# Optimization experiments

Measured on AMD Instinct MI355X. Metric: run time of the kernel, lower is better.

The kernel has to match this reference:

```python
import jax, jax.numpy as jnp
import numpy as np

B, L, D = 2048, 200, 128
ITEM_D, USER_D, CAT_D, DUR_D = 64, 64, 32, 16
N_USERS, N_ITEMS, N_CAT, N_DUR = 100000, 100000, 1000, 10
UDENSE, IDENSE = 25, 3
CONCAT = USER_D + ITEM_D + CAT_D + DUR_D + UDENSE + IDENSE + D  # 332
MLP1, MLP2 = 256, 128


def setup_inputs() -> dict:
    key = jax.random.key(0)
    ks = jax.random.split(key, 24)
    f = jax.random.normal
    hist_table = 0.01 * f(ks[0], (N_ITEMS + 1, D), dtype=jnp.float32)
    hist_table = hist_table.at[0].set(0.0)  # padding_idx=0
    return {
        'user_id': jax.random.randint(ks[1], (B,), 0, N_USERS, dtype=jnp.int32),
        'item_id': jax.random.randint(ks[2], (B,), 0, N_ITEMS, dtype=jnp.int32),
        'item_category': jax.random.randint(ks[3], (B,), 0, N_CAT, dtype=jnp.int32),
        'item_dur_bkt': jax.random.randint(ks[4], (B,), 0, N_DUR, dtype=jnp.int32),
        'history_seq': jax.random.randint(ks[5], (B, L), 0, N_ITEMS + 1, dtype=jnp.int32),
        'user_dense': f(ks[6], (B, UDENSE), dtype=jnp.float32),
        'item_dense': f(ks[7], (B, IDENSE), dtype=jnp.float32),
        'user_table': 0.01 * f(ks[8], (N_USERS, USER_D), dtype=jnp.float32),
        'item_table': 0.01 * f(ks[9], (N_ITEMS, ITEM_D), dtype=jnp.float32),
        'cat_table': 0.01 * f(ks[10], (N_CAT, CAT_D), dtype=jnp.float32),
        'dur_table': 0.01 * f(ks[11], (N_DUR, DUR_D), dtype=jnp.float32),
        'hist_table': hist_table,
        'target_proj_W': f(ks[12], (D, ITEM_D), dtype=jnp.float32) / np.sqrt(ITEM_D).astype(np.float32),
        'gru_Wi': f(ks[13], (3 * D, D), dtype=jnp.float32) / np.sqrt(D).astype(np.float32),
        'gru_Wh': f(ks[14], (3 * D, D), dtype=jnp.float32) / np.sqrt(D).astype(np.float32),
        'gru_bi': jnp.zeros((3 * D,), jnp.float32),
        'gru_bh': jnp.zeros((3 * D,), jnp.float32),
        'au_Wr': f(ks[15], (D, 2 * D), dtype=jnp.float32) / np.sqrt(2 * D).astype(np.float32),
        'au_br': jnp.zeros((D,), jnp.float32),
        'au_Wu': f(ks[16], (D, 2 * D), dtype=jnp.float32) / np.sqrt(2 * D).astype(np.float32),
        'au_bu': jnp.zeros((D,), jnp.float32),
        'au_Wh': f(ks[17], (D, 2 * D), dtype=jnp.float32) / np.sqrt(2 * D).astype(np.float32),
        'au_bh': jnp.zeros((D,), jnp.float32),
        'mlp_W1': f(ks[18], (MLP1, CONCAT), dtype=jnp.float32) / np.sqrt(CONCAT).astype(np.float32),
        'mlp_b1': jnp.zeros((MLP1,), jnp.float32),
        'mlp_W2': f(ks[19], (MLP2, MLP1), dtype=jnp.float32) / np.sqrt(MLP1).astype(np.float32),
        'mlp_b2': jnp.zeros((MLP2,), jnp.float32),
        'mlp_W3': f(ks[20], (1, MLP2), dtype=jnp.float32) / np.sqrt(MLP2).astype(np.float32),
        'mlp_b3': jnp.zeros((1,), jnp.float32),
    }


def _dien_fwd(user_id, item_id, item_category, item_dur_bkt, history_seq,
              user_dense, item_dense, user_table, item_table, cat_table,
              dur_table, hist_table, target_proj_W, gru_Wi, gru_Wh, gru_bi,
              gru_bh, au_Wr, au_br, au_Wu, au_bu, au_Wh, au_bh,
              mlp_W1, mlp_b1, mlp_W2, mlp_b2, mlp_W3, mlp_b3):
    mask = history_seq > 0                      # (B, L) bool, True = real item
    hist_emb = hist_table[history_seq]          # (B, L, D)

    # ---- InterestExtractor: torch nn.GRU (eval mode, dropout off) ----
    gi = jnp.einsum('bld,ed->ble', hist_emb, gru_Wi) + gru_bi  # (B, L, 3D)

    def gru_step(h, gi_t):
        gh = h @ gru_Wh.T + gru_bh
        i_r, i_z, i_n = jnp.split(gi_t, 3, axis=-1)
        h_r, h_z, h_n = jnp.split(gh, 3, axis=-1)
        r = jax.nn.sigmoid(i_r + h_r)
        z = jax.nn.sigmoid(i_z + h_z)
        n = jnp.tanh(i_n + r * h_n)
        h_new = (1.0 - z) * n + z * h
        return h_new, h_new

    h0 = jnp.zeros((hist_emb.shape[0], D), hist_emb.dtype)
    _, hs = jax.lax.scan(gru_step, h0, jnp.swapaxes(gi, 0, 1))
    h_states = jnp.swapaxes(hs, 0, 1)           # (B, L, D)

    # ---- Target-aware attention scores ----
    i_emb = item_table[item_id]                  # (B, ITEM_D)
    target = i_emb @ target_proj_W.T             # (B, D)
    scores = jnp.einsum('bld,bd->bl', h_states, target) / np.float32(np.sqrt(D))
    scores = jnp.where(mask, scores, jnp.float32(-1e9))
    attn = jax.nn.softmax(scores, axis=-1)       # (B, L)

    # ---- InterestEvolving: AUGRU scan over L timesteps ----
    def augru_step(h, inputs):
        x_t, e_t, m_t = inputs                   # (B,D), (B,), (B,)
        comb = jnp.concatenate([x_t, h], axis=-1)
        r = jax.nn.sigmoid(comb @ au_Wr.T + au_br)
        u = jax.nn.sigmoid(comb @ au_Wu.T + au_bu)
        u_prime = e_t[:, None] * u
        h_tilde = jnp.tanh(jnp.concatenate([x_t, r * h], axis=-1) @ au_Wh.T + au_bh)
        h_new = (1.0 - u_prime) * h + u_prime * h_tilde
        valid = m_t[:, None].astype(h.dtype)
        return valid * h_new + (1.0 - valid) * h, None

    xs = (jnp.swapaxes(h_states, 0, 1), attn.T, mask.T)
    evolved, _ = jax.lax.scan(augru_step, jnp.zeros_like(h0), xs)  # (B, D)

    # ---- Final MLP head ----
    x = jnp.concatenate([
        user_table[user_id], i_emb, cat_table[item_category],
        dur_table[item_dur_bkt], user_dense, item_dense, evolved], axis=-1)
    h1 = jax.nn.relu(x @ mlp_W1.T + mlp_b1)
    h2 = jax.nn.relu(h1 @ mlp_W2.T + mlp_b2)
    logit = (h2 @ mlp_W3.T + mlp_b3)[:, 0]
    return jax.nn.sigmoid(logit)                 # (B,)


def reference(user_id, item_id, item_category, item_dur_bkt, history_seq,
              user_dense, item_dense, user_table, item_table, cat_table,
              dur_table, hist_table, target_proj_W, gru_Wi, gru_Wh, gru_bi,
              gru_bh, au_Wr, au_br, au_Wu, au_bu, au_Wh, au_bh,
              mlp_W1, mlp_b1, mlp_W2, mlp_b2, mlp_W3, mlp_b3):
    return _dien_fwd(user_id, item_id, item_category, item_dur_bkt, history_seq,
                     user_dense, item_dense, user_table, item_table, cat_table,
                     dur_table, hist_table, target_proj_W, gru_Wi, gru_Wh, gru_bi,
                     gru_bh, au_Wr, au_br, au_Wu, au_bu, au_Wh, au_bh,
                     mlp_W1, mlp_b1, mlp_W2, mlp_b2, mlp_W3, mlp_b3)
```

## Files before the change

### kernel.cpp

```cpp
#include <hip/hip_runtime.h>
#include <cstdint>
#include <cstddef>

#define BB    2048
#define LL    200
#define GR    8
#define MR    8

typedef __attribute__((ext_vector_type(4))) float f32x4;
typedef __attribute__((ext_vector_type(8))) short s16x8;

__device__ __forceinline__ float fastrcp(float x) { return __builtin_amdgcn_rcpf(x); }
__device__ __forceinline__ float sigmf(float x) { return fastrcp(1.f + __expf(-x)); }
__device__ __forceinline__ float tanh2(float x) {
    return __builtin_fmaf(2.f, fastrcp(1.f + __expf(-2.f * x)), -1.f);
}
__device__ __forceinline__ float dot4(float4 a, float4 b) {
    return a.x * b.x + a.y * b.y + a.z * b.z + a.w * b.w;
}
__device__ __forceinline__ float4 ld4(const float* p) { return *(const float4*)p; }

__device__ __forceinline__ unsigned short f2bf(float f) {
    union { float f; unsigned u; } v; v.f = f;
    unsigned r = (v.u + 0x7FFFu + ((v.u >> 16) & 1u)) >> 16;
    return (unsigned short)r;
}
__device__ __forceinline__ float bf2f(unsigned short b) {
    unsigned u = ((unsigned)b) << 16;
    union { unsigned u; float f; } v; v.u = u;
    return v.f;
}
__device__ __forceinline__ s16x8 pack8g(const float* p) {
    float4 a = ld4(p), b = ld4(p + 4);
    s16x8 o;
    o[0] = (short)f2bf(a.x); o[1] = (short)f2bf(a.y);
    o[2] = (short)f2bf(a.z); o[3] = (short)f2bf(a.w);
    o[4] = (short)f2bf(b.x); o[5] = (short)f2bf(b.y);
    o[6] = (short)f2bf(b.z); o[7] = (short)f2bf(b.w);
    return o;
}
#define MFMA(a, b, c) __builtin_amdgcn_mfma_f32_16x16x32_bf16((a), (b), (c), 0, 0, 0)

#define BAR() do { \
    asm volatile("s_waitcnt lgkmcnt(0)" ::: "memory"); \
    __builtin_amdgcn_sched_barrier(0); \
    __builtin_amdgcn_s_barrier(); \
    __builtin_amdgcn_sched_barrier(0); \
} while (0)

#define RED2(A, O0, O1) { \
    float s2_ = __shfl(A[2], srcl), s3_ = __shfl(A[3], srcl); \
    O0 = hi ? s2_ : A[0]; O1 = hi ? s3_ : A[1]; \
}

__global__ __launch_bounds__(256) void cvt_hist(const float* __restrict__ src,
                                                unsigned short* __restrict__ dst, int n8) {
    int i = blockIdx.x * 256 + threadIdx.x;
    if (i < n8) *(s16x8*)(dst + (size_t)i * 8) = pack8g(src + (size_t)i * 8);
}

__global__ void transpose_kernel(const float* __restrict__ src, float* __restrict__ dst,
                                 int rows, int cols) {
    int k = blockIdx.x;
    for (int j = threadIdx.x; j < rows; j += blockDim.x)
        dst[(size_t)k * rows + j] = src[(size_t)j * cols + k];
}

__global__ __launch_bounds__(128) void target_kernel(
    const int* __restrict__ item_id, const float* __restrict__ item_table,
    const float* __restrict__ projW, float* __restrict__ target) {
    __shared__ float ie[64];
    int b = blockIdx.x, d = threadIdx.x;
    if (d < 64) ie[d] = item_table[(size_t)item_id[b] * 64 + d];
    __syncthreads();
    float acc = 0.f;
    const float* w = projW + (size_t)d * 64;
#pragma unroll
    for (int k = 0; k < 64; k += 4) acc += dot4(ld4(&ie[k]), ld4(w + k));
    target[(size_t)b * 128 + d] = acc;
}

__global__ __launch_bounds__(512, 2) void gru_v4(
    const int* __restrict__ hseq, const unsigned short* __restrict__ hist_bf,
    const float* __restrict__ Wi, const float* __restrict__ Wh,
    const float* __restrict__ bi, const float* __restrict__ bh,
    unsigned short* __restrict__ h_bf) {
    __shared__ alignas(16) unsigned short xf[2][2048];
    __shared__ alignas(16) unsigned short hf[2][2048];
    __shared__ int sq[GR * LL];
    const int tid = threadIdx.x;
    const int w = tid >> 6, lane = tid & 63;
    const int b0 = blockIdx.x * GR;
    const int cb = (w << 4) | (lane & 15);
    const int kc_ = cb >> 5, kq_ = (cb >> 3) & 3, jj = cb & 7;
    const int srcl = lane & 31;
    const bool hi = lane >= 32;
    const int rowb = ((lane & 31) >> 4) * 4 + (hi ? 2 : 0);
    s16x8 wir[4], wiz[4], win[4], whr[4], whz[4], whn[4];
    {
        int c = lane & 15, kg = (lane >> 4) * 8;
#pragma unroll
        for (int kc = 0; kc < 4; ++kc) {
            int ko = kc * 32 + kg;
            wir[kc] = pack8g(Wi + (size_t)(w * 16 + c) * 128 + ko);
            wiz[kc] = pack8g(Wi + (size_t)(128 + w * 16 + c) * 128 + ko);
            win[kc] = pack8g(Wi + (size_t)(256 + w * 16 + c) * 128 + ko);
            whr[kc] = pack8g(Wh + (size_t)(w * 16 + c) * 128 + ko);
            whz[kc] = pack8g(Wh + (size_t)(128 + w * 16 + c) * 128 + ko);
            whn[kc] = pack8g(Wh + (size_t)(256 + w * 16 + c) * 128 + ko);
        }
    }
    const float bi_r = bi[cb], bi_z = bi[128 + cb], bi_n = bi[256 + cb];
    const float bh_r = bh[cb], bh_z = bh[128 + cb], bh_n = bh[256 + cb];
    float hold0 = 0.f, hold1 = 0.f;
    for (int i = tid; i < 2048; i += 512) {
        xf[0][i] = 0; xf[1][i] = 0; hf[0][i] = 0; hf[1][i] = 0;
    }
    for (int i = tid; i < GR * LL; i += 512)
        sq[i] = hseq[(size_t)(b0 + i / LL) * LL + i % LL];
    __syncthreads();
    s16x8 pA, pB;
    if (lane < 16) {
        int idx0 = sq[w * LL + 0];
        *(s16x8*)&xf[0][(((lane >> 2) * 64) + (lane & 3) * 16 + w) * 8] =
            *(const s16x8*)(hist_bf + (size_t)idx0 * 128 + lane * 8);
        int idx1 = sq[w * LL + 1];
        pA = *(const s16x8*)(hist_bf + (size_t)idx1 * 128 + lane * 8);
    }
    __syncthreads();

#define GSTEP(TT, RD, CUR, NXT) { \
    const int tt = (TT); \
    if (lane < 16) { \
        *(s16x8*)&xf[RD ^ 1][(((lane >> 2) * 64) + (lane & 3) * 16 + w) * 8] = CUR; \
        int nidx = sq[w * LL + (tt + 2 < LL ? tt + 2 : LL - 1)]; \
        NXT = *(const s16x8*)(hist_bf + (size_t)nidx * 128 + lane * 8); \
    } \
    f32x4 ir = {0,0,0,0}, iz = {0,0,0,0}, in_ = {0,0,0,0}; \
    f32x4 hr = {0,0,0,0}, hz = {0,0,0,0}, hn_ = {0,0,0,0}; \
    _Pragma("unroll") for (int kc = 0; kc < 4; ++kc) { \
        s16x8 xa = *(const s16x8*)&xf[RD][(kc * 64 + lane) * 8]; \
        s16x8 ha = *(const s16x8*)&hf[RD][(kc * 64 + lane) * 8]; \
        ir = MFMA(xa, wir[kc], ir);  hr = MFMA(ha, whr[kc], hr); \
        iz = MFMA(xa, wiz[kc], iz);  hz = MFMA(ha, whz[kc], hz); \
        in_ = MFMA(xa, win[kc], in_); hn_ = MFMA(ha, whn[kc], hn_); \
    } \
    float xr0, xr1, xz0, xz1, xn0, xn1, yr0, yr1, yz0, yz1, yn0, yn1; \
    RED2(ir, xr0, xr1); RED2(iz, xz0, xz1); RED2(in_, xn0, xn1); \
    RED2(hr, yr0, yr1); RED2(hz, yz0, yz1); RED2(hn_, yn0, yn1); \
    { \
        float r = sigmf(xr0 + bi_r + yr0 + bh_r); \
        float z = sigmf(xz0 + bi_z + yz0 + bh_z); \
        float n = tanh2(xn0 + bi_n + r * (yn0 + bh_n)); \
        float hv = (1.f - z) * n + z * hold0; hold0 = hv; \
        unsigned short hb = f2bf(hv); \
        h_bf[((size_t)(b0 + rowb) * LL + tt) * 128 + cb] = hb; \
        hf[RD ^ 1][(kc_ * 64 + kq_ * 16 + rowb) * 8 + jj] = (short)hb; \
    } \
    { \
        float r = sigmf(xr1 + bi_r + yr1 + bh_r); \
        float z = sigmf(xz1 + bi_z + yz1 + bh_z); \
        float n = tanh2(xn1 + bi_n + r * (yn1 + bh_n)); \
        float hv = (1.f - z) * n + z * hold1; hold1 = hv; \
        unsigned short hb = f2bf(hv); \
        h_bf[((size_t)(b0 + rowb + 1) * LL + tt) * 128 + cb] = hb; \
        hf[RD ^ 1][(kc_ * 64 + kq_ * 16 + rowb + 1) * 8 + jj] = (short)hb; \
    } \
    BAR(); \
}

    for (int t2 = 0; t2 < LL / 2; ++t2) {
        GSTEP(2 * t2,     0, pA, pB);
        GSTEP(2 * t2 + 1, 1, pB, pA);
    }
#undef GSTEP
}

__global__ __launch_bounds__(256) void score_softmax(
    const unsigned short* __restrict__ h_bf, const float* __restrict__ target,
    const int* __restrict__ hseq, float* __restrict__ attn) {
    __shared__ float tg[128];
    __shared__ float rbuf[8];
    const int b = blockIdx.x, tid = threadIdx.x;
    const int wv = tid >> 6, lane = tid & 63;
    if (tid < 128) tg[tid] = target[(size_t)b * 128 + tid];
    __syncthreads();
    float v = -3.0e38f;
    if (tid < LL) {
        const unsigned short* hp = h_bf + ((size_t)b * LL + tid) * 128;
        float acc = 0.f;
#pragma unroll
        for (int k = 0; k < 128; k += 8) {
            s16x8 hv = *(const s16x8*)(hp + k);
#pragma unroll
            for (int j = 0; j < 8; ++j)
                acc = __builtin_fmaf(bf2f((unsigned short)hv[j]), tg[k + j], acc);
        }
        v = (hseq[(size_t)b * LL + tid] > 0) ? acc * 0.08838834764831845f : -1e9f;
    }
    float mx = v;
    for (int off = 1; off < 64; off <<= 1) mx = fmaxf(mx, __shfl_xor(mx, off));
    if (lane == 0) rbuf[wv] = mx;
    __syncthreads();
    mx = fmaxf(fmaxf(rbuf[0], rbuf[1]), fmaxf(rbuf[2], rbuf[3]));
    float e = (tid < LL) ? __expf(v - mx) : 0.f;
    float s = e;
    for (int off = 1; off < 64; off <<= 1) s += __shfl_xor(s, off);
    if (lane == 0) rbuf[4 + wv] = s;
    __syncthreads();
    s = rbuf[4] + rbuf[5] + rbuf[6] + rbuf[7];
    if (tid < LL) attn[(size_t)b * LL + tid] = e / s;
}

__global__ __launch_bounds__(512, 2) void augru_v4(
    const unsigned short* __restrict__ h_bf, const float* __restrict__ attn,
    const int* __restrict__ hseq,
    const float* __restrict__ Wr, const float* __restrict__ Wu,
    const float* __restrict__ Wht,
    const float* __restrict__ br, const float* __restrict__ bu,
    const float* __restrict__ bh, float* __restrict__ evolved) {
    __shared__ alignas(16) unsigned short xf[2][2048];
    __shared__ alignas(16) unsigned short hf[2][2048];
    __shared__ alignas(16) unsigned short rhf[2048];
    __shared__ float attl[GR * LL];
    __shared__ float mskl[GR * LL];
    const int tid = threadIdx.x;
    const int w = tid >> 6, lane = tid & 63;
    const int b0 = blockIdx.x * GR;
    const int cb = (w << 4) | (lane & 15);
    const int kc_ = cb >> 5, kq_ = (cb >> 3) & 3, jj = cb & 7;
    const int srcl = lane & 31;
    const bool hi = lane >= 32;
    const int rowb = ((lane & 31) >> 4) * 4 + (hi ? 2 : 0);
    s16x8 wr_[8], wu_[8], wx_[4], wh_[4];
    {
        int c = lane & 15, kg = (lane >> 4) * 8;
        int r0 = w * 16 + c;
#pragma unroll
        for (int kc = 0; kc < 8; ++kc) {
            wr_[kc] = pack8g(Wr + (size_t)r0 * 256 + kc * 32 + kg);
            wu_[kc] = pack8g(Wu + (size_t)r0 * 256 + kc * 32 + kg);
        }
#pragma unroll
        for (int kc = 0; kc < 4; ++kc) {
            wx_[kc] = pack8g(Wht + (size_t)r0 * 256 + kc * 32 + kg);
            wh_[kc] = pack8g(Wht + (size_t)r0 * 256 + 128 + kc * 32 + kg);
        }
    }
    const float br_c = br[cb], bu_c = bu[cb], bh_c = bh[cb];
    float hold0 = 0.f, hold1 = 0.f;
    for (int i = tid; i < 2048; i += 512) {
        xf[0][i] = 0; xf[1][i] = 0; hf[0][i] = 0; hf[1][i] = 0; rhf[i] = 0;
    }
    for (int i = tid; i < GR * LL; i += 512) {
        int r = i / LL, t = i % LL;
        attl[i] = attn[(size_t)(b0 + r) * LL + t];
        mskl[i] = (hseq[(size_t)(b0 + r) * LL + t] > 0) ? 1.f : 0.f;
    }
    __syncthreads();
    s16x8 pA, pB;
    if (lane < 16) {
        *(s16x8*)&xf[0][(((lane >> 2) * 64) + (lane & 3) * 16 + w) * 8] =
            *(const s16x8*)(h_bf + ((size_t)(b0 + w) * LL + 0) * 128 + lane * 8);
        pA = *(const s16x8*)(h_bf + ((size_t)(b0 + w) * LL + 1) * 128 + lane * 8);
    }
    __syncthreads();

#define ASTEP(TT, RD, CUR, NXT) { \
    const int tt = (TT); \
    if (lane < 16) { \
        *(s16x8*)&xf[RD ^ 1][(((lane >> 2) * 64) + (lane & 3) * 16 + w) * 8] = CUR; \
        int nt = tt + 2 < LL ? tt + 2 : LL - 1; \
        NXT = *(const s16x8*)(h_bf + ((size_t)(b0 + w) * LL + nt) * 128 + lane * 8); \
    } \
    f32x4 ar = {0,0,0,0}, au = {0,0,0,0}, ax = {0,0,0,0}; \
    _Pragma("unroll") for (int kc = 0; kc < 4; ++kc) { \
        s16x8 xa = *(const s16x8*)&xf[RD][(kc * 64 + lane) * 8]; \
        s16x8 ha = *(const s16x8*)&hf[RD][(kc * 64 + lane) * 8]; \
        ar = MFMA(xa, wr_[kc], ar); ar = MFMA(ha, wr_[kc + 4], ar); \
        au = MFMA(xa, wu_[kc], au); au = MFMA(ha, wu_[kc + 4], au); \
        ax = MFMA(xa, wx_[kc], ax); \
    } \
    { \
        float a0, a1; \
        RED2(ar, a0, a1); \
        float r0 = sigmf(a0 + br_c), r1 = sigmf(a1 + br_c); \
        rhf[(kc_ * 64 + kq_ * 16 + rowb) * 8 + jj] = (short)f2bf(r0 * hold0); \
        rhf[(kc_ * 64 + kq_ * 16 + rowb + 1) * 8 + jj] = (short)f2bf(r1 * hold1); \
    } \
    BAR(); \
    f32x4 ah = {0,0,0,0}; \
    _Pragma("unroll") for (int kc = 0; kc < 4; ++kc) { \
        s16x8 ra = *(const s16x8*)&rhf[(kc * 64 + lane) * 8]; \
        ah = MFMA(ra, wh_[kc], ah); \
    } \
    { \
        float u0, u1, x0, x1, g0, g1; \
        RED2(au, u0, u1); RED2(ax, x0, x1); RED2(ah, g0, g1); \
        float uu0 = sigmf(u0 + bu_c), uu1 = sigmf(u1 + bu_c); \
        float up0 = attl[rowb * LL + tt] * uu0; \
        float up1 = attl[(rowb + 1) * LL + tt] * uu1; \
        float ht0 = tanh2(x0 + g0 + bh_c), ht1 = tanh2(x1 + g1 + bh_c); \
        float hv0 = (1.f - up0) * hold0 + up0 * ht0; \
        float hv1 = (1.f - up1) * hold1 + up1 * ht1; \
        hold0 = mskl[rowb * LL + tt] > 0.5f ? hv0 : hold0; \
        hold1 = mskl[(rowb + 1) * LL + tt] > 0.5f ? hv1 : hold1; \
        hf[RD ^ 1][(kc_ * 64 + kq_ * 16 + rowb) * 8 + jj] = (short)f2bf(hold0); \
        hf[RD ^ 1][(kc_ * 64 + kq_ * 16 + rowb + 1) * 8 + jj] = (short)f2bf(hold1); \
    } \
    BAR(); \
}

    for (int t2 = 0; t2 < LL / 2; ++t2) {
        ASTEP(2 * t2,     0, pA, pB);
        ASTEP(2 * t2 + 1, 1, pB, pA);
    }
#undef ASTEP
    evolved[(size_t)(b0 + rowb) * 128 + cb] = hold0;
    evolved[(size_t)(b0 + rowb + 1) * 128 + cb] = hold1;
}

__global__ __launch_bounds__(256) void mlp_kernel(
    const int* __restrict__ user_id, const int* __restrict__ item_id,
    const int* __restrict__ item_cat, const int* __restrict__ item_dur,
    const float* __restrict__ user_dense, const float* __restrict__ item_dense,
    const float* __restrict__ user_table, const float* __restrict__ item_table,
    const float* __restrict__ cat_table, const float* __restrict__ dur_table,
    const float* __restrict__ evolved,
    const float* __restrict__ W1t, const float* __restrict__ b1,
    const float* __restrict__ W2t, const float* __restrict__ b2,
    const float* __restrict__ W3, const float* __restrict__ b3,
    float* __restrict__ out) {
    __shared__ float Xs[MR][332];
    __shared__ float h1s[MR][256];
    __shared__ float h2s[MR][128];
    __shared__ int ids[4][MR];
    const int tid = threadIdx.x;
    const int b0 = blockIdx.x * MR;
    if (tid < MR) {
        ids[0][tid] = user_id[b0 + tid];
        ids[1][tid] = item_id[b0 + tid];
        ids[2][tid] = item_cat[b0 + tid];
        ids[3][tid] = item_dur[b0 + tid];
    }
    __syncthreads();
    for (int i = tid; i < MR * 332; i += 256) {
        int r = i / 332, c = i % 332;
        int b = b0 + r;
        float v;
        if (c < 64) v = user_table[(size_t)ids[0][r] * 64 + c];
        else if (c < 128) v = item_table[(size_t)ids[1][r] * 64 + (c - 64)];
        else if (c < 160) v = cat_table[(size_t)ids[2][r] * 32 + (c - 128)];
        else if (c < 176) v = dur_table[(size_t)ids[3][r] * 16 + (c - 160)];
        else if (c < 201) v = user_dense[(size_t)b * 25 + (c - 176)];
        else if (c < 204) v = item_dense[(size_t)b * 3 + (c - 201)];
        else v = evolved[(size_t)b * 128 + (c - 204)];
        Xs[r][c] = v;
    }
    __syncthreads();
    {
        float acc[MR] = {0, 0, 0, 0, 0, 0, 0, 0};
        for (int k = 0; k < 332; ++k) {
            float ww = W1t[(size_t)k * 256 + tid];
#pragma unroll
            for (int r = 0; r < MR; ++r) acc[r] += Xs[r][k] * ww;
        }
        float bb = b1[tid];
#pragma unroll
        for (int r = 0; r < MR; ++r) h1s[r][tid] = fmaxf(acc[r] + bb, 0.f);
    }
    __syncthreads();
    if (tid < 128) {
        float acc[MR] = {0, 0, 0, 0, 0, 0, 0, 0};
        for (int k = 0; k < 256; ++k) {
            float ww = W2t[(size_t)k * 128 + tid];
#pragma unroll
            for (int r = 0; r < MR; ++r) acc[r] += h1s[r][k] * ww;
        }
        float bb = b2[tid];
#pragma unroll
        for (int r = 0; r < MR; ++r) h2s[r][tid] = fmaxf(acc[r] + bb, 0.f);
    }
    __syncthreads();
    {
        int r = tid >> 5, j = tid & 31;
        float p = 0.f;
#pragma unroll
        for (int m = 0; m < 4; ++m) p += h2s[r][j + 32 * m] * W3[j + 32 * m];
        p += __shfl_xor(p, 16);
        p += __shfl_xor(p, 8);
        p += __shfl_xor(p, 4);
        p += __shfl_xor(p, 2);
        p += __shfl_xor(p, 1);
        if (j == 0) out[b0 + r] = 1.f / (1.f + __expf(-(p + b3[0])));
    }
}

extern "C" void kernel_launch(void* const* d_in, const int* in_sizes, int n_in,
                              void* d_out, int out_size, void* d_ws, size_t ws_size,
                              hipStream_t stream) {
    const int* user_id = (const int*)d_in[0];
    const int* item_id = (const int*)d_in[1];
    const int* item_cat = (const int*)d_in[2];
    const int* item_dur = (const int*)d_in[3];
    const int* hseq = (const int*)d_in[4];
    const float* user_dense = (const float*)d_in[5];
    const float* item_dense = (const float*)d_in[6];
    const float* user_table = (const float*)d_in[7];
    const float* item_table = (const float*)d_in[8];
    const float* cat_table = (const float*)d_in[9];
    const float* dur_table = (const float*)d_in[10];
    const float* hist_table = (const float*)d_in[11];
    const float* projW = (const float*)d_in[12];
    const float* gWi = (const float*)d_in[13];
    const float* gWh = (const float*)d_in[14];
    const float* gbi = (const float*)d_in[15];
    const float* gbh = (const float*)d_in[16];
    const float* aWr = (const float*)d_in[17];
    const float* abr = (const float*)d_in[18];
    const float* aWu = (const float*)d_in[19];
    const float* abu = (const float*)d_in[20];
    const float* aWh = (const float*)d_in[21];
    const float* abh = (const float*)d_in[22];
    const float* mW1 = (const float*)d_in[23];
    const float* mb1 = (const float*)d_in[24];
    const float* mW2 = (const float*)d_in[25];
    const float* mb2 = (const float*)d_in[26];
    const float* mW3 = (const float*)d_in[27];
    const float* mb3 = (const float*)d_in[28];
    float* out = (float*)d_out;

    float* ws = (float*)d_ws;
    float* target = ws;
    unsigned short* h_bf = (unsigned short*)(ws + 262144);
    float* attn = ws + 262144 + 26214400;
    float* evolved = attn + 409600;
    float* W1t = evolved + 262144;
    float* W2t = W1t + 84992;
    unsigned short* hist_bf = (unsigned short*)(W2t + 32768);

    const int n8 = 100001 * 16;
    hipLaunchKernelGGL(cvt_hist, dim3((n8 + 255) / 256), dim3(256), 0, stream,
                       hist_table, hist_bf, n8);
    hipLaunchKernelGGL(transpose_kernel, dim3(332), dim3(256), 0, stream, mW1, W1t, 256, 332);
    hipLaunchKernelGGL(transpose_kernel, dim3(256), dim3(128), 0, stream, mW2, W2t, 128, 256);
    hipLaunchKernelGGL(target_kernel, dim3(2048), dim3(128), 0, stream,
                       item_id, item_table, projW, target);
    hipLaunchKernelGGL(gru_v4, dim3(BB / GR), dim3(512), 0, stream,
                       hseq, hist_bf, gWi, gWh, gbi, gbh, h_bf);
    hipLaunchKernelGGL(score_softmax, dim3(BB), dim3(256), 0, stream,
                       h_bf, target, hseq, attn);
    hipLaunchKernelGGL(augru_v4, dim3(BB / GR), dim3(512), 0, stream,
                       h_bf, attn, hseq, aWr, aWu, aWh, abr, abu, abh, evolved);
    hipLaunchKernelGGL(mlp_kernel, dim3(BB / MR), dim3(256), 0, stream,
                       user_id, item_id, item_cat, item_dur, user_dense, item_dense,
                       user_table, item_table, cat_table, dur_table, evolved,
                       W1t, mb1, W2t, mb2, mW3, mb3, out);
}
```

Before: 473.3 us.

## Halve rows per block in GRU/AUGRU recurrences and drop cross-lane reduction

Each block of the GRU and AUGRU recurrent kernels now handles 4 batch rows instead of 8. That doubles the grid to 512 blocks and raises the launch-bounds occupancy hint from 2 to 4 blocks per CU. Lanes 0-15 now read all four MFMA output rows directly, so the shuffle-based RED2 reduction goes away, and input and hidden projections for the r/z gates are accumulated into the same MFMA accumulator. The aim is more parallelism across CUs for the latency-bound sequential loop, at the cost of MFMA tiles running half-empty (rows 4-15 are padding) and fewer lanes doing the elementwise work.

```diff
diff --git a/kernel.cpp b/kernel.cpp
--- a/kernel.cpp
+++ b/kernel.cpp
@@ -4,7 +4,7 @@
 
 #define BB    2048
 #define LL    200
-#define GR    8
+#define GR    4
 #define MR    8
 
 typedef __attribute__((ext_vector_type(4))) float f32x4;
@@ -48,11 +48,6 @@
     __builtin_amdgcn_sched_barrier(0); \
 } while (0)
 
-#define RED2(A, O0, O1) { \
-    float s2_ = __shfl(A[2], srcl), s3_ = __shfl(A[3], srcl); \
-    O0 = hi ? s2_ : A[0]; O1 = hi ? s3_ : A[1]; \
-}
-
 __global__ __launch_bounds__(256) void cvt_hist(const float* __restrict__ src,
                                                 unsigned short* __restrict__ dst, int n8) {
     int i = blockIdx.x * 256 + threadIdx.x;
@@ -80,7 +75,7 @@
     target[(size_t)b * 128 + d] = acc;
 }
 
-__global__ __launch_bounds__(512, 2) void gru_v4(
+__global__ __launch_bounds__(512, 4) void gru_v5(
     const int* __restrict__ hseq, const unsigned short* __restrict__ hist_bf,
     const float* __restrict__ Wi, const float* __restrict__ Wh,
     const float* __restrict__ bi, const float* __restrict__ bh,
@@ -93,9 +88,6 @@
     const int b0 = blockIdx.x * GR;
     const int cb = (w << 4) | (lane & 15);
     const int kc_ = cb >> 5, kq_ = (cb >> 3) & 3, jj = cb & 7;
-    const int srcl = lane & 31;
-    const bool hi = lane >= 32;
-    const int rowb = ((lane & 31) >> 4) * 4 + (hi ? 2 : 0);
     s16x8 wir[4], wiz[4], win[4], whr[4], whz[4], whn[4];
     {
         int c = lane & 15, kg = (lane >> 4) * 8;
@@ -110,9 +102,10 @@
             whn[kc] = pack8g(Wh + (size_t)(256 + w * 16 + c) * 128 + ko);
         }
     }
-    const float bi_r = bi[cb], bi_z = bi[128 + cb], bi_n = bi[256 + cb];
-    const float bh_r = bh[cb], bh_z = bh[128 + cb], bh_n = bh[256 + cb];
-    float hold0 = 0.f, hold1 = 0.f;
+    const float b_r = bi[cb] + bh[cb];
+    const float b_z = bi[128 + cb] + bh[128 + cb];
+    const float bi_n = bi[256 + cb], bh_n = bh[256 + cb];
+    float hold[4] = {0, 0, 0, 0};
     for (int i = tid; i < 2048; i += 512) {
         xf[0][i] = 0; xf[1][i] = 0; hf[0][i] = 0; hf[1][i] = 0;
     }
@@ -120,7 +113,7 @@
         sq[i] = hseq[(size_t)(b0 + i / LL) * LL + i % LL];
     __syncthreads();
     s16x8 pA, pB;
-    if (lane < 16) {
+    if (w < GR && lane < 16) {
         int idx0 = sq[w * LL + 0];
         *(s16x8*)&xf[0][(((lane >> 2) * 64) + (lane & 3) * 16 + w) * 8] =
             *(const s16x8*)(hist_bf + (size_t)idx0 * 128 + lane * 8);
@@ -131,40 +124,29 @@
 
 #define GSTEP(TT, RD, CUR, NXT) { \
     const int tt = (TT); \
-    if (lane < 16) { \
+    if (w < GR && lane < 16) { \
         *(s16x8*)&xf[RD ^ 1][(((lane >> 2) * 64) + (lane & 3) * 16 + w) * 8] = CUR; \
         int nidx = sq[w * LL + (tt + 2 < LL ? tt + 2 : LL - 1)]; \
         NXT = *(const s16x8*)(hist_bf + (size_t)nidx * 128 + lane * 8); \
     } \
-    f32x4 ir = {0,0,0,0}, iz = {0,0,0,0}, in_ = {0,0,0,0}; \
-    f32x4 hr = {0,0,0,0}, hz = {0,0,0,0}, hn_ = {0,0,0,0}; \
+    f32x4 ar = {0,0,0,0}, az = {0,0,0,0}, ain = {0,0,0,0}, ahn = {0,0,0,0}; \
     _Pragma("unroll") for (int kc = 0; kc < 4; ++kc) { \
         s16x8 xa = *(const s16x8*)&xf[RD][(kc * 64 + lane) * 8]; \
         s16x8 ha = *(const s16x8*)&hf[RD][(kc * 64 + lane) * 8]; \
-        ir = MFMA(xa, wir[kc], ir);  hr = MFMA(ha, whr[kc], hr); \
-        iz = MFMA(xa, wiz[kc], iz);  hz = MFMA(ha, whz[kc], hz); \
-        in_ = MFMA(xa, win[kc], in_); hn_ = MFMA(ha, whn[kc], hn_); \
-    } \
-    float xr0, xr1, xz0, xz1, xn0, xn1, yr0, yr1, yz0, yz1, yn0, yn1; \
-    RED2(ir, xr0, xr1); RED2(iz, xz0, xz1); RED2(in_, xn0, xn1); \
-    RED2(hr, yr0, yr1); RED2(hz, yz0, yz1); RED2(hn_, yn0, yn1); \
-    { \
-        float r = sigmf(xr0 + bi_r + yr0 + bh_r); \
-        float z = sigmf(xz0 + bi_z + yz0 + bh_z); \
-        float n = tanh2(xn0 + bi_n + r * (yn0 + bh_n)); \
-        float hv = (1.f - z) * n + z * hold0; hold0 = hv; \
-        unsigned short hb = f2bf(hv); \
-        h_bf[((size_t)(b0 + rowb) * LL + tt) * 128 + cb] = hb; \
-        hf[RD ^ 1][(kc_ * 64 + kq_ * 16 + rowb) * 8 + jj] = (short)hb; \
-    } \
-    { \
-        float r = sigmf(xr1 + bi_r + yr1 + bh_r); \
-        float z = sigmf(xz1 + bi_z + yz1 + bh_z); \
-        float n = tanh2(xn1 + bi_n + r * (yn1 + bh_n)); \
-        float hv = (1.f - z) * n + z * hold1; hold1 = hv; \
-        unsigned short hb = f2bf(hv); \
-        h_bf[((size_t)(b0 + rowb + 1) * LL + tt) * 128 + cb] = hb; \
-        hf[RD ^ 1][(kc_ * 64 + kq_ * 16 + rowb + 1) * 8 + jj] = (short)hb; \
+        ar = MFMA(xa, wir[kc], ar); ar = MFMA(ha, whr[kc], ar); \
+        az = MFMA(xa, wiz[kc], az); az = MFMA(ha, whz[kc], az); \
+        ain = MFMA(xa, win[kc], ain); ahn = MFMA(ha, whn[kc], ahn); \
+    } \
+    if (lane < 16) { \
+        _Pragma("unroll") for (int q = 0; q < 4; ++q) { \
+            float r = sigmf(ar[q] + b_r); \
+            float z = sigmf(az[q] + b_z); \
+            float n = tanh2(ain[q] + bi_n + r * (ahn[q] + bh_n)); \
+            float hv = (1.f - z) * n + z * hold[q]; hold[q] = hv; \
+            unsigned short hb = f2bf(hv); \
+            h_bf[((size_t)(b0 + q) * LL + tt) * 128 + cb] = hb; \
+            hf[RD ^ 1][(kc_ * 64 + kq_ * 16 + q) * 8 + jj] = (short)hb; \
+        } \
     } \
     BAR(); \
 }
@@ -212,7 +194,7 @@
     if (tid < LL) attn[(size_t)b * LL + tid] = e / s;
 }
 
-__global__ __launch_bounds__(512, 2) void augru_v4(
+__global__ __launch_bounds__(512, 4) void augru_v5(
     const unsigned short* __restrict__ h_bf, const float* __restrict__ attn,
     const int* __restrict__ hseq,
     const float* __restrict__ Wr, const float* __restrict__ Wu,
@@ -229,9 +211,6 @@
     const int b0 = blockIdx.x * GR;
     const int cb = (w << 4) | (lane & 15);
     const int kc_ = cb >> 5, kq_ = (cb >> 3) & 3, jj = cb & 7;
-    const int srcl = lane & 31;
-    const bool hi = lane >= 32;
-    const int rowb = ((lane & 31) >> 4) * 4 + (hi ? 2 : 0);
     s16x8 wr_[8], wu_[8], wx_[4], wh_[4];
     {
         int c = lane & 15, kg = (lane >> 4) * 8;
@@ -248,7 +227,7 @@
         }
     }
     const float br_c = br[cb], bu_c = bu[cb], bh_c = bh[cb];
-    float hold0 = 0.f, hold1 = 0.f;
+    float hold[4] = {0, 0, 0, 0};
     for (int i = tid; i < 2048; i += 512) {
         xf[0][i] = 0; xf[1][i] = 0; hf[0][i] = 0; hf[1][i] = 0; rhf[i] = 0;
     }
@@ -259,7 +238,7 @@
     }
     __syncthreads();
     s16x8 pA, pB;
-    if (lane < 16) {
+    if (w < GR && lane < 16) {
         *(s16x8*)&xf[0][(((lane >> 2) * 64) + (lane & 3) * 16 + w) * 8] =
             *(const s16x8*)(h_bf + ((size_t)(b0 + w) * LL + 0) * 128 + lane * 8);
         pA = *(const s16x8*)(h_bf + ((size_t)(b0 + w) * LL + 1) * 128 + lane * 8);
@@ -268,7 +247,7 @@
 
 #define ASTEP(TT, RD, CUR, NXT) { \
     const int tt = (TT); \
-    if (lane < 16) { \
+    if (w < GR && lane < 16) { \
         *(s16x8*)&xf[RD ^ 1][(((lane >> 2) * 64) + (lane & 3) * 16 + w) * 8] = CUR; \
         int nt = tt + 2 < LL ? tt + 2 : LL - 1; \
         NXT = *(const s16x8*)(h_bf + ((size_t)(b0 + w) * LL + nt) * 128 + lane * 8); \
@@ -281,12 +260,11 @@
         au = MFMA(xa, wu_[kc], au); au = MFMA(ha, wu_[kc + 4], au); \
         ax = MFMA(xa, wx_[kc], ax); \
     } \
-    { \
-        float a0, a1; \
-        RED2(ar, a0, a1); \
-        float r0 = sigmf(a0 + br_c), r1 = sigmf(a1 + br_c); \
-        rhf[(kc_ * 64 + kq_ * 16 + rowb) * 8 + jj] = (short)f2bf(r0 * hold0); \
-        rhf[(kc_ * 64 + kq_ * 16 + rowb + 1) * 8 + jj] = (short)f2bf(r1 * hold1); \
+    if (lane < 16) { \
+        _Pragma("unroll") for (int q = 0; q < 4; ++q) { \
+            float r = sigmf(ar[q] + br_c); \
+            rhf[(kc_ * 64 + kq_ * 16 + q) * 8 + jj] = (short)f2bf(r * hold[q]); \
+        } \
     } \
     BAR(); \
     f32x4 ah = {0,0,0,0}; \
@@ -294,19 +272,15 @@
         s16x8 ra = *(const s16x8*)&rhf[(kc * 64 + lane) * 8]; \
         ah = MFMA(ra, wh_[kc], ah); \
     } \
-    { \
-        float u0, u1, x0, x1, g0, g1; \
-        RED2(au, u0, u1); RED2(ax, x0, x1); RED2(ah, g0, g1); \
-        float uu0 = sigmf(u0 + bu_c), uu1 = sigmf(u1 + bu_c); \
-        float up0 = attl[rowb * LL + tt] * uu0; \
-        float up1 = attl[(rowb + 1) * LL + tt] * uu1; \
-        float ht0 = tanh2(x0 + g0 + bh_c), ht1 = tanh2(x1 + g1 + bh_c); \
-        float hv0 = (1.f - up0) * hold0 + up0 * ht0; \
-        float hv1 = (1.f - up1) * hold1 + up1 * ht1; \
-        hold0 = mskl[rowb * LL + tt] > 0.5f ? hv0 : hold0; \
-        hold1 = mskl[(rowb + 1) * LL + tt] > 0.5f ? hv1 : hold1; \
-        hf[RD ^ 1][(kc_ * 64 + kq_ * 16 + rowb) * 8 + jj] = (short)f2bf(hold0); \
-        hf[RD ^ 1][(kc_ * 64 + kq_ * 16 + rowb + 1) * 8 + jj] = (short)f2bf(hold1); \
+    if (lane < 16) { \
+        _Pragma("unroll") for (int q = 0; q < 4; ++q) { \
+            float u = sigmf(au[q] + bu_c); \
+            float up = attl[q * LL + tt] * u; \
+            float ht = tanh2(ax[q] + ah[q] + bh_c); \
+            float hv = (1.f - up) * hold[q] + up * ht; \
+            hold[q] = mskl[q * LL + tt] > 0.5f ? hv : hold[q]; \
+            hf[RD ^ 1][(kc_ * 64 + kq_ * 16 + q) * 8 + jj] = (short)f2bf(hold[q]); \
+        } \
     } \
     BAR(); \
 }
@@ -316,8 +290,11 @@
         ASTEP(2 * t2 + 1, 1, pB, pA);
     }
 #undef ASTEP
-    evolved[(size_t)(b0 + rowb) * 128 + cb] = hold0;
-    evolved[(size_t)(b0 + rowb + 1) * 128 + cb] = hold1;
+    if (lane < 16) {
+#pragma unroll
+        for (int q = 0; q < 4; ++q)
+            evolved[(size_t)(b0 + q) * 128 + cb] = hold[q];
+    }
 }
 
 __global__ __launch_bounds__(256) void mlp_kernel(
@@ -446,11 +423,11 @@
     hipLaunchKernelGGL(transpose_kernel, dim3(256), dim3(128), 0, stream, mW2, W2t, 128, 256);
     hipLaunchKernelGGL(target_kernel, dim3(2048), dim3(128), 0, stream,
                        item_id, item_table, projW, target);
-    hipLaunchKernelGGL(gru_v4, dim3(BB / GR), dim3(512), 0, stream,
+    hipLaunchKernelGGL(gru_v5, dim3(BB / GR), dim3(512), 0, stream,
                        hseq, hist_bf, gWi, gWh, gbi, gbh, h_bf);
     hipLaunchKernelGGL(score_softmax, dim3(BB), dim3(256), 0, stream,
                        h_bf, target, hseq, attn);
-    hipLaunchKernelGGL(augru_v4, dim3(BB / GR), dim3(512), 0, stream,
+    hipLaunchKernelGGL(augru_v5, dim3(BB / GR), dim3(512), 0, stream,
                        h_bf, attn, hseq, aWr, aWu, aWh, abr, abu, abh, evolved);
     hipLaunchKernelGGL(mlp_kernel, dim3(BB / MR), dim3(256), 0, stream,
                        user_id, item_id, item_cat, item_dur, user_dense, item_dense,
```

Result: slower. 1.220 ms (+157.7%).

## Store GRU hidden states in block-tiled fragment layout and batch score/softmax per 8 rows

Applied to the files above, without the earlier changes.

The GRU kernel now writes hidden states as coalesced 16-byte chunks copied from the shared-memory fragment buffer, one step behind, in a per-block tiled layout. Previously each lane did scattered 2-byte global stores. The r and z MFMA accumulators are fused (input and hidden products summed in one accumulator) to cut reductions and registers. Score/softmax and AUGRU are rewritten to consume the new tiled layout, with softmax handling 8 batch rows per block. This adds layout coupling between the three kernels and an extra shared-memory read per step in the GRU.

```diff
diff --git a/kernel.cpp b/kernel.cpp
--- a/kernel.cpp
+++ b/kernel.cpp
@@ -80,11 +80,11 @@
     target[(size_t)b * 128 + d] = acc;
 }
 
-__global__ __launch_bounds__(512, 2) void gru_v4(
+__global__ __launch_bounds__(512, 2) void gru_v6(
     const int* __restrict__ hseq, const unsigned short* __restrict__ hist_bf,
     const float* __restrict__ Wi, const float* __restrict__ Wh,
     const float* __restrict__ bi, const float* __restrict__ bh,
-    unsigned short* __restrict__ h_bf) {
+    unsigned short* __restrict__ h2) {
     __shared__ alignas(16) unsigned short xf[2][2048];
     __shared__ alignas(16) unsigned short hf[2][2048];
     __shared__ int sq[GR * LL];
@@ -96,6 +96,8 @@
     const int srcl = lane & 31;
     const bool hi = lane >= 32;
     const int rowb = ((lane & 31) >> 4) * 4 + (hi ? 2 : 0);
+    const int fs = ((tid >> 5) * 64 + ((tid >> 3) & 3) * 16 + (tid & 7)) * 8;
+    unsigned short* const h2p = h2 + (size_t)blockIdx.x * (LL * 1024);
     s16x8 wir[4], wiz[4], win[4], whr[4], whz[4], whn[4];
     {
         int c = lane & 15, kg = (lane >> 4) * 8;
@@ -110,8 +112,9 @@
             whn[kc] = pack8g(Wh + (size_t)(256 + w * 16 + c) * 128 + ko);
         }
     }
-    const float bi_r = bi[cb], bi_z = bi[128 + cb], bi_n = bi[256 + cb];
-    const float bh_r = bh[cb], bh_z = bh[128 + cb], bh_n = bh[256 + cb];
+    const float b_r = bi[cb] + bh[cb];
+    const float b_z = bi[128 + cb] + bh[128 + cb];
+    const float bi_n = bi[256 + cb], bh_n = bh[256 + cb];
     float hold0 = 0.f, hold1 = 0.f;
     for (int i = tid; i < 2048; i += 512) {
         xf[0][i] = 0; xf[1][i] = 0; hf[0][i] = 0; hf[1][i] = 0;
@@ -121,11 +124,11 @@
     __syncthreads();
     s16x8 pA, pB;
     if (lane < 16) {
-        int idx0 = sq[w * LL + 0];
+        unsigned o0 = (unsigned)sq[w * LL + 0] << 7;
         *(s16x8*)&xf[0][(((lane >> 2) * 64) + (lane & 3) * 16 + w) * 8] =
-            *(const s16x8*)(hist_bf + (size_t)idx0 * 128 + lane * 8);
-        int idx1 = sq[w * LL + 1];
-        pA = *(const s16x8*)(hist_bf + (size_t)idx1 * 128 + lane * 8);
+            *(const s16x8*)(hist_bf + o0 + lane * 8);
+        unsigned o1 = (unsigned)sq[w * LL + 1] << 7;
+        pA = *(const s16x8*)(hist_bf + o1 + lane * 8);
     }
     __syncthreads();
 
@@ -133,38 +136,33 @@
     const int tt = (TT); \
     if (lane < 16) { \
         *(s16x8*)&xf[RD ^ 1][(((lane >> 2) * 64) + (lane & 3) * 16 + w) * 8] = CUR; \
-        int nidx = sq[w * LL + (tt + 2 < LL ? tt + 2 : LL - 1)]; \
-        NXT = *(const s16x8*)(hist_bf + (size_t)nidx * 128 + lane * 8); \
-    } \
-    f32x4 ir = {0,0,0,0}, iz = {0,0,0,0}, in_ = {0,0,0,0}; \
-    f32x4 hr = {0,0,0,0}, hz = {0,0,0,0}, hn_ = {0,0,0,0}; \
+        unsigned no = (unsigned)sq[w * LL + (tt + 2 < LL ? tt + 2 : LL - 1)] << 7; \
+        NXT = *(const s16x8*)(hist_bf + no + lane * 8); \
+    } \
+    if (tt > 0 && tid < 128) {   \
+        s16x8 hv = *(const s16x8*)&hf[RD][fs]; \
+        *(s16x8*)(h2p + (unsigned)(tt - 1) * 1024 + tid * 8) = hv; \
+    } \
+    f32x4 ar = {0,0,0,0}, az = {0,0,0,0}, ain = {0,0,0,0}, ahn = {0,0,0,0}; \
     _Pragma("unroll") for (int kc = 0; kc < 4; ++kc) { \
         s16x8 xa = *(const s16x8*)&xf[RD][(kc * 64 + lane) * 8]; \
         s16x8 ha = *(const s16x8*)&hf[RD][(kc * 64 + lane) * 8]; \
-        ir = MFMA(xa, wir[kc], ir);  hr = MFMA(ha, whr[kc], hr); \
-        iz = MFMA(xa, wiz[kc], iz);  hz = MFMA(ha, whz[kc], hz); \
-        in_ = MFMA(xa, win[kc], in_); hn_ = MFMA(ha, whn[kc], hn_); \
-    } \
-    float xr0, xr1, xz0, xz1, xn0, xn1, yr0, yr1, yz0, yz1, yn0, yn1; \
-    RED2(ir, xr0, xr1); RED2(iz, xz0, xz1); RED2(in_, xn0, xn1); \
-    RED2(hr, yr0, yr1); RED2(hz, yz0, yz1); RED2(hn_, yn0, yn1); \
+        ar = MFMA(xa, wir[kc], ar); ar = MFMA(ha, whr[kc], ar); \
+        az = MFMA(xa, wiz[kc], az); az = MFMA(ha, whz[kc], az); \
+        ain = MFMA(xa, win[kc], ain); ahn = MFMA(ha, whn[kc], ahn); \
+    } \
     { \
-        float r = sigmf(xr0 + bi_r + yr0 + bh_r); \
-        float z = sigmf(xz0 + bi_z + yz0 + bh_z); \
-        float n = tanh2(xn0 + bi_n + r * (yn0 + bh_n)); \
-        float hv = (1.f - z) * n + z * hold0; hold0 = hv; \
-        unsigned short hb = f2bf(hv); \
-        h_bf[((size_t)(b0 + rowb) * LL + tt) * 128 + cb] = hb; \
-        hf[RD ^ 1][(kc_ * 64 + kq_ * 16 + rowb) * 8 + jj] = (short)hb; \
-    } \
-    { \
-        float r = sigmf(xr1 + bi_r + yr1 + bh_r); \
-        float z = sigmf(xz1 + bi_z + yz1 + bh_z); \
-        float n = tanh2(xn1 + bi_n + r * (yn1 + bh_n)); \
-        float hv = (1.f - z) * n + z * hold1; hold1 = hv; \
-        unsigned short hb = f2bf(hv); \
-        h_bf[((size_t)(b0 + rowb + 1) * LL + tt) * 128 + cb] = hb; \
-        hf[RD ^ 1][(kc_ * 64 + kq_ * 16 + rowb + 1) * 8 + jj] = (short)hb; \
+        float r0x, r1x, z0x, z1x, ni0, ni1, nh0, nh1; \
+        RED2(ar, r0x, r1x); RED2(az, z0x, z1x); \
+        RED2(ain, ni0, ni1); RED2(ahn, nh0, nh1); \
+        float r0 = sigmf(r0x + b_r), z0 = sigmf(z0x + b_z); \
+        float n0 = tanh2(ni0 + bi_n + r0 * (nh0 + bh_n)); \
+        float hv0 = (1.f - z0) * n0 + z0 * hold0; hold0 = hv0; \
+        hf[RD ^ 1][(kc_ * 64 + kq_ * 16 + rowb) * 8 + jj] = (short)f2bf(hv0); \
+        float r1 = sigmf(r1x + b_r), z1 = sigmf(z1x + b_z); \
+        float n1 = tanh2(ni1 + bi_n + r1 * (nh1 + bh_n)); \
+        float hv1 = (1.f - z1) * n1 + z1 * hold1; hold1 = hv1; \
+        hf[RD ^ 1][(kc_ * 64 + kq_ * 16 + rowb + 1) * 8 + jj] = (short)f2bf(hv1); \
     } \
     BAR(); \
 }
@@ -174,46 +172,76 @@
         GSTEP(2 * t2 + 1, 1, pB, pA);
     }
 #undef GSTEP
-}
-
-__global__ __launch_bounds__(256) void score_softmax(
-    const unsigned short* __restrict__ h_bf, const float* __restrict__ target,
+    if (tid < 128) {
+        s16x8 hv = *(const s16x8*)&hf[0][fs];
+        *(s16x8*)(h2p + (unsigned)(LL - 1) * 1024 + tid * 8) = hv;
+    }
+}
+
+__global__ __launch_bounds__(512) void score_softmax2(
+    const unsigned short* __restrict__ h2, const float* __restrict__ target,
     const int* __restrict__ hseq, float* __restrict__ attn) {
-    __shared__ float tg[128];
-    __shared__ float rbuf[8];
-    const int b = blockIdx.x, tid = threadIdx.x;
+    __shared__ float tg[8][128];
+    __shared__ float sA[8][LL];
+    __shared__ float sB[8][LL];
+    const int tid = threadIdx.x;
+    const int blk = blockIdx.x;
+    const int b0 = blk * 8;
+    {
+        int r = tid >> 6, d2 = (tid & 63) * 2;
+        tg[r][d2] = target[(size_t)(b0 + r) * 128 + d2];
+        tg[r][d2 + 1] = target[(size_t)(b0 + r) * 128 + d2 + 1];
+    }
+    __syncthreads();
+    const unsigned short* const hp = h2 + (size_t)blk * (LL * 1024);
+    const int g = tid >> 7;
+    const int u = tid & 127;
+    const int row = u & 7;
+    const int d0 = (u >> 5) * 32 + ((u >> 3) & 3) * 8;
+    const int half = u >> 6;
+    for (int t = g; t < LL; t += 4) {
+        s16x8 hv = *(const s16x8*)(hp + (unsigned)t * 1024 + u * 8);
+        float acc = 0.f;
+#pragma unroll
+        for (int j = 0; j < 8; ++j)
+            acc = __builtin_fmaf(bf2f((unsigned short)hv[j]), tg[row][d0 + j], acc);
+        acc += __shfl_xor(acc, 8);
+        acc += __shfl_xor(acc, 16);
+        acc += __shfl_xor(acc, 32);
+        if ((u & 63) < 8) { (half ? sB : sA)[row][t] = acc; }
+    }
+    __syncthreads();
     const int wv = tid >> 6, lane = tid & 63;
-    if (tid < 128) tg[tid] = target[(size_t)b * 128 + tid];
-    __syncthreads();
-    float v = -3.0e38f;
-    if (tid < LL) {
-        const unsigned short* hp = h_bf + ((size_t)b * LL + tid) * 128;
-        float acc = 0.f;
-#pragma unroll
-        for (int k = 0; k < 128; k += 8) {
-            s16x8 hv = *(const s16x8*)(hp + k);
-#pragma unroll
-            for (int j = 0; j < 8; ++j)
-                acc = __builtin_fmaf(bf2f((unsigned short)hv[j]), tg[k + j], acc);
-        }
-        v = (hseq[(size_t)b * LL + tid] > 0) ? acc * 0.08838834764831845f : -1e9f;
-    }
-    float mx = v;
+    float v[4];
+#pragma unroll
+    for (int m = 0; m < 4; ++m) {
+        int t = lane + 64 * m;
+        if (t < LL) {
+            float s = (sA[wv][t] + sB[wv][t]) * 0.08838834764831845f;
+            v[m] = (hseq[(size_t)(b0 + wv) * LL + t] > 0) ? s : -1e9f;
+        } else
+            v[m] = -3.0e38f;
+    }
+    float mx = fmaxf(fmaxf(v[0], v[1]), fmaxf(v[2], v[3]));
     for (int off = 1; off < 64; off <<= 1) mx = fmaxf(mx, __shfl_xor(mx, off));
-    if (lane == 0) rbuf[wv] = mx;
-    __syncthreads();
-    mx = fmaxf(fmaxf(rbuf[0], rbuf[1]), fmaxf(rbuf[2], rbuf[3]));
-    float e = (tid < LL) ? __expf(v - mx) : 0.f;
-    float s = e;
+    float s = 0.f;
+#pragma unroll
+    for (int m = 0; m < 4; ++m) {
+        int t = lane + 64 * m;
+        v[m] = (t < LL) ? __expf(v[m] - mx) : 0.f;
+        s += v[m];
+    }
     for (int off = 1; off < 64; off <<= 1) s += __shfl_xor(s, off);
-    if (lane == 0) rbuf[4 + wv] = s;
-    __syncthreads();
-    s = rbuf[4] + rbuf[5] + rbuf[6] + rbuf[7];
-    if (tid < LL) attn[(size_t)b * LL + tid] = e / s;
-}
-
-__global__ __launch_bounds__(512, 2) void augru_v4(
-    const unsigned short* __restrict__ h_bf, const float* __restrict__ attn,
+    float inv = fastrcp(s);
+#pragma unroll
+    for (int m = 0; m < 4; ++m) {
+        int t = lane + 64 * m;
+        if (t < LL) attn[(size_t)(b0 + wv) * LL + t] = v[m] * inv;
+    }
+}
+
+__global__ __launch_bounds__(512, 2) void augru_v6(
+    const unsigned short* __restrict__ h2, const float* __restrict__ attn,
     const int* __restrict__ hseq,
     const float* __restrict__ Wr, const float* __restrict__ Wu,
     const float* __restrict__ Wht,
@@ -232,6 +260,8 @@
     const int srcl = lane & 31;
     const bool hi = lane >= 32;
     const int rowb = ((lane & 31) >> 4) * 4 + (hi ? 2 : 0);
+    const int fs = ((tid >> 5) * 64 + ((tid >> 3) & 3) * 16 + (tid & 7)) * 8;
+    const unsigned short* const h2p = h2 + (size_t)blockIdx.x * (LL * 1024);
     s16x8 wr_[8], wu_[8], wx_[4], wh_[4];
     {
         int c = lane & 15, kg = (lane >> 4) * 8;
@@ -259,19 +289,18 @@
     }
     __syncthreads();
     s16x8 pA, pB;
-    if (lane < 16) {
-        *(s16x8*)&xf[0][(((lane >> 2) * 64) + (lane & 3) * 16 + w) * 8] =
-            *(const s16x8*)(h_bf + ((size_t)(b0 + w) * LL + 0) * 128 + lane * 8);
-        pA = *(const s16x8*)(h_bf + ((size_t)(b0 + w) * LL + 1) * 128 + lane * 8);
+    if (tid < 128) {
+        *(s16x8*)&xf[0][fs] = *(const s16x8*)(h2p + tid * 8);
+        pA = *(const s16x8*)(h2p + 1024 + tid * 8);
     }
     __syncthreads();
 
 #define ASTEP(TT, RD, CUR, NXT) { \
     const int tt = (TT); \
-    if (lane < 16) { \
-        *(s16x8*)&xf[RD ^ 1][(((lane >> 2) * 64) + (lane & 3) * 16 + w) * 8] = CUR; \
-        int nt = tt + 2 < LL ? tt + 2 : LL - 1; \
-        NXT = *(const s16x8*)(h_bf + ((size_t)(b0 + w) * LL + nt) * 128 + lane * 8); \
+    if (tid < 128) { \
+        *(s16x8*)&xf[RD ^ 1][fs] = CUR; \
+        unsigned nt = (tt + 2 < LL ? tt + 2 : LL - 1); \
+        NXT = *(const s16x8*)(h2p + nt * 1024 + tid * 8); \
     } \
     f32x4 ar = {0,0,0,0}, au = {0,0,0,0}, ax = {0,0,0,0}; \
     _Pragma("unroll") for (int kc = 0; kc < 4; ++kc) { \
@@ -432,7 +461,7 @@
 
     float* ws = (float*)d_ws;
     float* target = ws;
-    unsigned short* h_bf = (unsigned short*)(ws + 262144);
+    unsigned short* h2 = (unsigned short*)(ws + 262144);
     float* attn = ws + 262144 + 26214400;
     float* evolved = attn + 409600;
     float* W1t = evolved + 262144;
@@ -446,12 +475,12 @@
     hipLaunchKernelGGL(transpose_kernel, dim3(256), dim3(128), 0, stream, mW2, W2t, 128, 256);
     hipLaunchKernelGGL(target_kernel, dim3(2048), dim3(128), 0, stream,
                        item_id, item_table, projW, target);
-    hipLaunchKernelGGL(gru_v4, dim3(BB / GR), dim3(512), 0, stream,
-                       hseq, hist_bf, gWi, gWh, gbi, gbh, h_bf);
-    hipLaunchKernelGGL(score_softmax, dim3(BB), dim3(256), 0, stream,
-                       h_bf, target, hseq, attn);
-    hipLaunchKernelGGL(augru_v4, dim3(BB / GR), dim3(512), 0, stream,
-                       h_bf, attn, hseq, aWr, aWu, aWh, abr, abu, abh, evolved);
+    hipLaunchKernelGGL(gru_v6, dim3(BB / GR), dim3(512), 0, stream,
+                       hseq, hist_bf, gWi, gWh, gbi, gbh, h2);
+    hipLaunchKernelGGL(score_softmax2, dim3(BB / 8), dim3(512), 0, stream,
+                       h2, target, hseq, attn);
+    hipLaunchKernelGGL(augru_v6, dim3(BB / GR), dim3(512), 0, stream,
+                       h2, attn, hseq, aWr, aWu, aWh, abr, abu, abh, evolved);
     hipLaunchKernelGGL(mlp_kernel, dim3(BB / MR), dim3(256), 0, stream,
                        user_id, item_id, item_cat, item_dur, user_dense, item_dense,
                        user_table, item_table, cat_table, dur_table, evolved,
```

New measurement: 450.5 us, median of 2. 1.05x faster.
